# Optimization experiments

Measured on AMD Instinct MI355X. Metric: run time of the kernel, lower is better.

The kernel has to match this reference:

```python
import jax, jax.numpy as jnp
import numpy as np

N_NODES = 100000
N_EDGES = 3200000
D_FEAT = 128
N1 = 128
N2 = 64
NUM_CLASSES = 10
NUM_GRAPHS = 256


def gcn_conv(x, edge_index, W, b, num_nodes):
    """PyG GCNConv: y = D^-1/2 (A+I) D^-1/2 (x W) + b, self-loops added."""
    src, dst = edge_index[0], edge_index[1]
    # degree including self-loop (edge weight 1)
    deg = jax.ops.segment_sum(jnp.ones_like(dst, dtype=x.dtype), dst,
                              num_segments=num_nodes) + 1.0
    dis = jnp.where(deg > 0, deg ** -0.5, 0.0)  # deg_inv_sqrt, [N]
    h = x @ W                                    # transform first, [N, out]
    norm = dis[src] * dis[dst]                   # [E]
    msg = h[src] * norm[:, None]                 # gather + scale, [E, out]
    agg = jax.ops.segment_sum(msg, dst, num_segments=num_nodes)
    agg = agg + h * (dis * dis)[:, None]         # self-loop contribution
    return agg + b


def global_mean_pool(x, batch, num_graphs):
    sums = jax.ops.segment_sum(x, batch, num_segments=num_graphs)
    cnt = jax.ops.segment_sum(jnp.ones((x.shape[0],), dtype=x.dtype), batch,
                              num_segments=num_graphs)
    return sums / jnp.maximum(cnt, 1.0)[:, None]


def setup_inputs() -> dict:
    key = jax.random.key(0)
    ks = jax.random.split(key, 8)
    x = jax.random.normal(ks[0], (N_NODES, D_FEAT), dtype=jnp.float32)
    edge_index = jax.random.randint(ks[1], (2, N_EDGES), 0, N_NODES, dtype=jnp.int64)
    batch = jnp.sort(jax.random.randint(ks[2], (N_NODES,), 0, NUM_GRAPHS, dtype=jnp.int64))
    W1 = jax.random.normal(ks[3], (D_FEAT, N1), dtype=jnp.float32) / np.sqrt(D_FEAT)
    b1 = jnp.zeros((N1,), dtype=jnp.float32)
    W2 = jax.random.normal(ks[4], (N1, N2), dtype=jnp.float32) / np.sqrt(N1)
    b2 = jnp.zeros((N2,), dtype=jnp.float32)
    Wfc = jax.random.normal(ks[5], (N2, NUM_CLASSES), dtype=jnp.float32) / np.sqrt(N2)
    bfc = jnp.zeros((NUM_CLASSES,), dtype=jnp.float32)
    return {"x": x, "edge_index": edge_index, "batch": batch,
            "W1": W1, "b1": b1, "W2": W2, "b2": b2,
            "Wfc": Wfc, "bfc": bfc, "num_graphs": NUM_GRAPHS}


def reference(x, edge_index, batch, W1, b1, W2, b2, Wfc, bfc, num_graphs):
    n = x.shape[0]
    h = gcn_conv(x, edge_index, W1, b1, n)
    h = jax.nn.relu(h)
    h = gcn_conv(h, edge_index, W2, b2, n)
    g = global_mean_pool(h, batch, num_graphs)   # [num_graphs, N2]
    # dropout is identity at inference
    return g @ Wfc + bfc                          # [num_graphs, num_classes]
```

## Files before the change

### kernel.cpp

```cpp
#include <hip/hip_runtime.h>
#include <math.h>

typedef unsigned int  u32;
typedef unsigned short u16;

#define TILE1 8192
#define BKW   256
#define CAP   9216

typedef __attribute__((ext_vector_type(8))) short bf16x8;
typedef __attribute__((ext_vector_type(4))) float f32x4;
typedef __attribute__((ext_vector_type(2))) float f32x2;
union frag_u { bf16x8 v; u32 u[4]; uint4 q; };

__device__ inline u32 bf16_rne(float f) {
    u32 u = __float_as_uint(f);
    return (u + 0x7FFFu + ((u >> 16) & 1u)) >> 16;
}
__device__ inline float bf_lo(u32 u) { return __uint_as_float(u << 16); }
__device__ inline float bf_hi(u32 u) { return __uint_as_float(u & 0xFFFF0000u); }

__device__ inline f32x2 up2(u32 u) {
    f32x2 t;
    t.x = __uint_as_float(u << 16);
    t.y = __uint_as_float(u & 0xFFFF0000u);
    return t;
}
__device__ inline void add8p(f32x2* a, uint4 q) {
    a[0] += up2(q.x); a[1] += up2(q.y); a[2] += up2(q.z); a[3] += up2(q.w);
}

__device__ inline u32 relu_pk(u32 v) {
    u32 s = v & 0x80008000u;
    u32 m = (s >> 15) * 0xFFFFu;
    return v & ~m;
}


__global__ __launch_bounds__(512) void k_part1(const int* __restrict__ ei,
                                               int* __restrict__ bucketCur,
                                               u32* __restrict__ tmp,
                                               int E, int N, int NBK) {
    __shared__ int hist[2048];
    __shared__ int base[512];
    const int tid = threadIdx.x;
    if (tid < NBK) {
        hist[tid] = 0; hist[512 + tid] = 0;
        hist[1024 + tid] = 0; hist[1536 + tid] = 0;
    }
    __syncthreads();

    const int rep = (tid & 3) << 9;
    const int t0 = blockIdx.x * TILE1;
    const int4* ei4s = (const int4*)ei;
    const int4* ei4d = (const int4*)(ei + E);
    const int q0 = t0 >> 2;
    const int QE = E >> 2;

    int sv[16], dv[16], key[16];
#pragma unroll
    for (int j = 0; j < 4; ++j) {
        int qi = q0 + j * 512 + tid;
        int4 s4 = make_int4(0, 0, 0, 0), d4 = make_int4(-1, -1, -1, -1);
        if (qi < QE) { s4 = ei4s[qi]; d4 = ei4d[qi]; }
        sv[4 * j + 0] = s4.x; dv[4 * j + 0] = d4.x;
        sv[4 * j + 1] = s4.y; dv[4 * j + 1] = d4.y;
        sv[4 * j + 2] = s4.z; dv[4 * j + 2] = d4.z;
        sv[4 * j + 3] = s4.w; dv[4 * j + 3] = d4.w;
    }
#pragma unroll
    for (int j = 0; j < 16; ++j) {
        key[j] = -1;
        if ((unsigned)dv[j] < (unsigned)N && (unsigned)sv[j] < (unsigned)N) {
            key[j] = dv[j] >> 8;
            atomicAdd(&hist[key[j] + rep], 1);
        }
    }
    __syncthreads();
    if (tid < NBK) {
        int tot = hist[tid] + hist[512 + tid] + hist[1024 + tid] + hist[1536 + tid];
        base[tid] = atomicAdd(&bucketCur[tid], tot);
        hist[tid] = 0;
    }
    __syncthreads();
#pragma unroll
    for (int j = 0; j < 16; ++j) {
        if (key[j] >= 0) {
            int slot = atomicAdd(&hist[key[j]], 1);
            int off = base[key[j]] + slot;
            if (off < CAP)
                tmp[(size_t)key[j] * CAP + off] =
                    ((u32)(dv[j] & 255) << 17) | (u32)sv[j];
        }
    }
}

__global__ __launch_bounds__(512) void k_part2(const int* __restrict__ bucketCnt,
                                               const u32* __restrict__ tmp,
                                               int* __restrict__ csr,
                                               int* __restrict__ rowptr,
                                               float* __restrict__ dis,
                                               int N, int NBK) {
    __shared__ int hist[256];
    __shared__ int ts[512];
    __shared__ int sStart;
    const int b = blockIdx.x;
    const int t = threadIdx.x;

    int myCnt = (t < NBK) ? bucketCnt[t] : 0;
    ts[t] = myCnt;
    __syncthreads();
    for (int off = 1; off < 512; off <<= 1) {
        int u = (t >= off) ? ts[t - off] : 0;
        __syncthreads();
        ts[t] += u;
        __syncthreads();
    }
    if (t == b) sStart = ts[t] - myCnt;
    if (b == 0 && t == NBK - 1) rowptr[N] = ts[t];
    __syncthreads();
    const int start = sStart;
    const int cnt = bucketCnt[b];
    const u32* src = tmp + (size_t)b * CAP;

    if (t < 256) hist[t] = 0;
    __syncthreads();
    for (int i = t; i < cnt; i += 512)
        atomicAdd(&hist[src[i] >> 17], 1);
    __syncthreads();

    int h = (t < 256) ? hist[t] : 0;
    ts[t] = h;
    __syncthreads();
    for (int off = 1; off < 512; off <<= 1) {
        int u = (t >= off) ? ts[t - off] : 0;
        __syncthreads();
        ts[t] += u;
        __syncthreads();
    }
    if (t < 256) hist[t] = ts[t] - h;
    __syncthreads();

    if (t < 256) {
        int gn = (b << 8) + t;
        if (gn < N) {
            int e0 = hist[t];
            int e1 = (t < 255) ? hist[t + 1] : cnt;
            rowptr[gn] = start + e0;
            dis[gn] = rsqrtf((float)(e1 - e0) + 1.0f);
        }
    }
    __syncthreads();

    for (int i = t; i < cnt; i += 512) {
        u32 v = src[i];
        int p = atomicAdd(&hist[v >> 17], 1);
        csr[start + p] = (int)(v & 0x1FFFFu);
    }
}


__global__ __launch_bounds__(256) void k_convW(
    const float* __restrict__ W1, const float* __restrict__ W2,
    u32* __restrict__ W1h, u32* __restrict__ W1l,
    u32* __restrict__ W2h, u32* __restrict__ W2l,
    int* __restrict__ bucketCur, int NBK)
{
    int idx = blockIdx.x * 256 + threadIdx.x;
    if (idx < NBK) bucketCur[idx] = 0;
    if (idx < 8192) {
        int n = idx >> 6, k = (idx & 63) * 2;
        float w0 = W1[k * 128 + n], w1 = W1[(k + 1) * 128 + n];
        u32 h0 = bf16_rne(w0), h1 = bf16_rne(w1);
        u32 l0 = bf16_rne(w0 - __uint_as_float(h0 << 16));
        u32 l1 = bf16_rne(w1 - __uint_as_float(h1 << 16));
        W1h[idx] = h0 | (h1 << 16);
        W1l[idx] = l0 | (l1 << 16);
    } else if (idx < 12288) {
        int i2 = idx - 8192;
        int n = i2 >> 6, k = (i2 & 63) * 2;
        float w0 = W2[k * 64 + n], w1 = W2[(k + 1) * 64 + n];
        u32 h0 = bf16_rne(w0), h1 = bf16_rne(w1);
        u32 l0 = bf16_rne(w0 - __uint_as_float(h0 << 16));
        u32 l1 = bf16_rne(w1 - __uint_as_float(h1 << 16));
        W2h[i2] = h0 | (h1 << 16);
        W2l[i2] = l0 | (l1 << 16);
    }
}


__global__ __launch_bounds__(256) void k_gemm1m(
    const float* __restrict__ X, const u32* __restrict__ Wh,
    const u32* __restrict__ Wl, const float* __restrict__ dis,
    u32* __restrict__ Hb, int M)
{
    __shared__ uint4 sW[4096];
    const int tid = threadIdx.x;
    const uint4* Wh4 = (const uint4*)Wh;
    const uint4* Wl4 = (const uint4*)Wl;
#pragma unroll
    for (int i = 0; i < 8; ++i) {
        int idx = tid + i * 256;
        int l = idx >> 4, j = idx & 15;
        int js = j ^ (l & 7);
        sW[l * 16 + js] = Wh4[idx];
        sW[2048 + l * 16 + js] = Wl4[idx];
    }
    __syncthreads();

    const int w = tid >> 6, lane = tid & 63;
    const int mrow = blockIdx.x * 128 + w * 32;
    const int m16 = lane & 15, quad = lane >> 4;

    frag_u Ah[2][4], Al[2][4];
#pragma unroll
    for (int t = 0; t < 2; ++t) {
        int gm = mrow + t * 16 + m16; if (gm >= M) gm = M - 1;
        const float* xr = X + (size_t)gm * 128;
#pragma unroll
        for (int kt = 0; kt < 4; ++kt) {
            int kb = kt * 32 + quad * 8;
            float4 xa = *(const float4*)(xr + kb);
            float4 xb = *(const float4*)(xr + kb + 4);
            float xe[8] = {xa.x, xa.y, xa.z, xa.w, xb.x, xb.y, xb.z, xb.w};
#pragma unroll
            for (int j = 0; j < 4; ++j) {
                u32 h0 = bf16_rne(xe[2 * j]),     h1 = bf16_rne(xe[2 * j + 1]);
                u32 l0 = bf16_rne(xe[2 * j]     - __uint_as_float(h0 << 16));
                u32 l1 = bf16_rne(xe[2 * j + 1] - __uint_as_float(h1 << 16));
                Ah[t][kt].u[j] = h0 | (h1 << 16);
                Al[t][kt].u[j] = l0 | (l1 << 16);
            }
        }
    }

    float dv[2][4];
#pragma unroll
    for (int t = 0; t < 2; ++t)
#pragma unroll
        for (int r = 0; r < 4; ++r) {
            int gR = mrow + t * 16 + quad * 4 + r;
            dv[t][r] = (gR < M) ? dis[gR] : 0.f;
        }

#pragma unroll
    for (int nt = 0; nt < 8; ++nt) {
        f32x4 acc0 = {0.f, 0.f, 0.f, 0.f};
        f32x4 acc1 = {0.f, 0.f, 0.f, 0.f};
        int l = nt * 16 + m16;
        int swz = l & 7;
#pragma unroll
        for (int kt = 0; kt < 4; ++kt) {
            frag_u Bh, Bl;
            int jb = (kt * 4 + quad) ^ swz;
            Bh.q = sW[l * 16 + jb];
            Bl.q = sW[2048 + l * 16 + jb];
            acc0 = __builtin_amdgcn_mfma_f32_16x16x32_bf16(Al[0][kt].v, Bh.v, acc0, 0, 0, 0);
            acc0 = __builtin_amdgcn_mfma_f32_16x16x32_bf16(Ah[0][kt].v, Bl.v, acc0, 0, 0, 0);
            acc0 = __builtin_amdgcn_mfma_f32_16x16x32_bf16(Ah[0][kt].v, Bh.v, acc0, 0, 0, 0);
            acc1 = __builtin_amdgcn_mfma_f32_16x16x32_bf16(Al[1][kt].v, Bh.v, acc1, 0, 0, 0);
            acc1 = __builtin_amdgcn_mfma_f32_16x16x32_bf16(Ah[1][kt].v, Bl.v, acc1, 0, 0, 0);
            acc1 = __builtin_amdgcn_mfma_f32_16x16x32_bf16(Ah[1][kt].v, Bh.v, acc1, 0, 0, 0);
        }
#pragma unroll
        for (int r = 0; r < 4; ++r) {
            float vs0 = acc0[r] * dv[0][r];
            float vo0 = __shfl_xor(vs0, 1, 64);
            float vs1 = acc1[r] * dv[1][r];
            float vo1 = __shfl_xor(vs1, 1, 64);
            if ((m16 & 1) == 0) {
                int gR0 = mrow + quad * 4 + r;
                if (gR0 < M)
                    Hb[(size_t)gR0 * 64 + nt * 8 + (m16 >> 1)] =
                        bf16_rne(vs0) | (bf16_rne(vo0) << 16);
                int gR1 = mrow + 16 + quad * 4 + r;
                if (gR1 < M)
                    Hb[(size_t)gR1 * 64 + nt * 8 + (m16 >> 1)] =
                        bf16_rne(vs1) | (bf16_rne(vo1) << 16);
            }
        }
    }
}


__global__ __launch_bounds__(256) void k_gemm2m(
    const u32* __restrict__ Xb, const u32* __restrict__ Wh,
    const u32* __restrict__ Wl, const float* __restrict__ dis,
    u32* __restrict__ Hb, int M)
{
    __shared__ uint4 sW[2176];
    const int tid = threadIdx.x;
    const uint4* Wh4 = (const uint4*)Wh;
    const uint4* Wl4 = (const uint4*)Wl;
#pragma unroll
    for (int i = 0; i < 4; ++i) {
        int idx = tid + i * 256;
        int l = idx >> 4, j = idx & 15;
        sW[l * 17 + j] = Wh4[l * 16 + j];
        sW[1088 + l * 17 + j] = Wl4[l * 16 + j];
    }
    __syncthreads();

    const int w = tid >> 6, lane = tid & 63;
    const int mrow = blockIdx.x * 128 + w * 32;
    const int m16 = lane & 15, quad = lane >> 4;

    const uint4* X4 = (const uint4*)Xb;
    frag_u A[2][4];
#pragma unroll
    for (int t = 0; t < 2; ++t) {
        int gm = mrow + t * 16 + m16; if (gm >= M) gm = M - 1;
#pragma unroll
        for (int kt = 0; kt < 4; ++kt) {
            A[t][kt].q = X4[(size_t)gm * 16 + kt * 4 + quad];
#pragma unroll
            for (int j = 0; j < 4; ++j) A[t][kt].u[j] = relu_pk(A[t][kt].u[j]);
        }
    }

    float dv[2][4];
#pragma unroll
    for (int t = 0; t < 2; ++t)
#pragma unroll
        for (int r = 0; r < 4; ++r) {
            int gR = mrow + t * 16 + quad * 4 + r;
            dv[t][r] = (gR < M) ? dis[gR] : 0.f;
        }

#pragma unroll
    for (int nt = 0; nt < 4; ++nt) {
        f32x4 acc0 = {0.f, 0.f, 0.f, 0.f};
        f32x4 acc1 = {0.f, 0.f, 0.f, 0.f};
        int l = nt * 16 + m16;
#pragma unroll
        for (int kt = 0; kt < 4; ++kt) {
            frag_u Bh, Bl;
            Bh.q = sW[l * 17 + kt * 4 + quad];
            Bl.q = sW[1088 + l * 17 + kt * 4 + quad];
            acc0 = __builtin_amdgcn_mfma_f32_16x16x32_bf16(A[0][kt].v, Bl.v, acc0, 0, 0, 0);
            acc0 = __builtin_amdgcn_mfma_f32_16x16x32_bf16(A[0][kt].v, Bh.v, acc0, 0, 0, 0);
            acc1 = __builtin_amdgcn_mfma_f32_16x16x32_bf16(A[1][kt].v, Bl.v, acc1, 0, 0, 0);
            acc1 = __builtin_amdgcn_mfma_f32_16x16x32_bf16(A[1][kt].v, Bh.v, acc1, 0, 0, 0);
        }
#pragma unroll
        for (int r = 0; r < 4; ++r) {
            float vs0 = acc0[r] * dv[0][r];
            float vo0 = __shfl_xor(vs0, 1, 64);
            float vs1 = acc1[r] * dv[1][r];
            float vo1 = __shfl_xor(vs1, 1, 64);
            if ((m16 & 1) == 0) {
                int gR0 = mrow + quad * 4 + r;
                if (gR0 < M)
                    Hb[(size_t)gR0 * 32 + nt * 8 + (m16 >> 1)] =
                        bf16_rne(vs0) | (bf16_rne(vo0) << 16);
                int gR1 = mrow + 16 + quad * 4 + r;
                if (gR1 < M)
                    Hb[(size_t)gR1 * 32 + nt * 8 + (m16 >> 1)] =
                        bf16_rne(vs1) | (bf16_rne(vo1) << 16);
            }
        }
    }
}


template <int SH, int POFF>
__global__ __launch_bounds__(256) void k_aggh(
    const int* __restrict__ rowptr, const int* __restrict__ csr,
    const float* __restrict__ dis, const u32* __restrict__ Hb,
    const float* __restrict__ bias, u32* __restrict__ AGGb, int n0, int n1)
{
    int gid = blockIdx.x * 256 + threadIdx.x;
    int n = n0 + (gid >> 3);
    int li = threadIdx.x & 7;
    if (n >= n1) return;
    int e = rowptr[n];
    int s1 = rowptr[n + 1];
    const float dn = dis[n];
    const char* hb = (const char*)Hb;
    const u32 off = (u32)(POFF + li * 16);

    f32x2 acc[4];
#pragma unroll
    for (int j = 0; j < 4; ++j) acc[j] = 0.f;

    for (; e + 8 <= s1; e += 8) {
        u32 b0 = (u32)csr[e + 0] << SH;
        u32 b1 = (u32)csr[e + 1] << SH;
        u32 b2 = (u32)csr[e + 2] << SH;
        u32 b3 = (u32)csr[e + 3] << SH;
        u32 b4 = (u32)csr[e + 4] << SH;
        u32 b5 = (u32)csr[e + 5] << SH;
        u32 b6 = (u32)csr[e + 6] << SH;
        u32 b7 = (u32)csr[e + 7] << SH;
        uint4 q0 = *(const uint4*)(hb + b0 + off);
        uint4 q1 = *(const uint4*)(hb + b1 + off);
        uint4 q2 = *(const uint4*)(hb + b2 + off);
        uint4 q3 = *(const uint4*)(hb + b3 + off);
        uint4 q4 = *(const uint4*)(hb + b4 + off);
        uint4 q5 = *(const uint4*)(hb + b5 + off);
        uint4 q6 = *(const uint4*)(hb + b6 + off);
        uint4 q7 = *(const uint4*)(hb + b7 + off);
        add8p(acc, q0); add8p(acc, q1); add8p(acc, q2); add8p(acc, q3);
        add8p(acc, q4); add8p(acc, q5); add8p(acc, q6); add8p(acc, q7);
    }
    for (; e + 2 <= s1; e += 2) {
        u32 b0 = (u32)csr[e + 0] << SH;
        u32 b1 = (u32)csr[e + 1] << SH;
        uint4 q0 = *(const uint4*)(hb + b0 + off);
        uint4 q1 = *(const uint4*)(hb + b1 + off);
        add8p(acc, q0); add8p(acc, q1);
    }
    if (e < s1) {
        u32 b0 = (u32)csr[e] << SH;
        uint4 q0 = *(const uint4*)(hb + b0 + off);
        add8p(acc, q0);
    }
    {
        uint4 q = *(const uint4*)(hb + ((u32)n << SH) + off);
        add8p(acc, q);
    }

    float4 b0 = ((const float4*)bias)[POFF / 8 + li * 2 + 0];
    float4 b1 = ((const float4*)bias)[POFF / 8 + li * 2 + 1];
    uint4 p;
    p.x = bf16_rne(fmaf(dn, acc[0].x, b0.x)) | (bf16_rne(fmaf(dn, acc[0].y, b0.y)) << 16);
    p.y = bf16_rne(fmaf(dn, acc[1].x, b0.z)) | (bf16_rne(fmaf(dn, acc[1].y, b0.w)) << 16);
    p.z = bf16_rne(fmaf(dn, acc[2].x, b1.x)) | (bf16_rne(fmaf(dn, acc[2].y, b1.y)) << 16);
    p.w = bf16_rne(fmaf(dn, acc[3].x, b1.z)) | (bf16_rne(fmaf(dn, acc[3].y, b1.w)) << 16);
    ((uint4*)AGGb)[(size_t)n * (1 << (SH - 4)) + POFF / 16 + li] = p;
}


__device__ inline int lower_bound(const int* __restrict__ b, int n, int v) {
    int lo = 0, hi = n;
    while (lo < hi) { int m = (lo + hi) >> 1; if (b[m] < v) lo = m + 1; else hi = m; }
    return lo;
}

__global__ __launch_bounds__(256) void k_poolfc(
    const int* __restrict__ batch, const u32* __restrict__ AGGb2,
    const float* __restrict__ Wfc, const float* __restrict__ bfc,
    float* __restrict__ out, int n)
{
    int g = blockIdx.x;
    int start = lower_bound(batch, n, g);
    int end   = lower_bound(batch, n, g + 1);
    int tid = threadIdx.x;
    int f = tid & 63, stripe = tid >> 6;
    int ui = f >> 1, hi = f & 1;
    float acc = 0.f;
    for (int i = start + stripe; i < end; i += 4) {
        u32 v = AGGb2[(size_t)i * 32 + ui];
        acc += hi ? bf_hi(v) : bf_lo(v);
    }
    __shared__ float red[256];
    __shared__ float mean[64];
    red[tid] = acc;
    __syncthreads();
    if (tid < 64) {
        float s = red[tid] + red[tid + 64] + red[tid + 128] + red[tid + 192];
        float c = (float)(end - start);
        mean[tid] = s / fmaxf(c, 1.0f);
    }
    __syncthreads();
    if (tid < 10) {
        float o = bfc[tid];
        for (int k = 0; k < 64; ++k)
            o = fmaf(mean[k], Wfc[k * 10 + tid], o);
        out[g * 10 + tid] = o;
    }
}


extern "C" void kernel_launch(void* const* d_in, const int* in_sizes, int n_in,
                              void* d_out, int out_size, void* d_ws, size_t ws_size,
                              hipStream_t stream)
{
    const float* x    = (const float*)d_in[0];
    const int*   ei   = (const int*)d_in[1];
    const int*   batch= (const int*)d_in[2];
    const float* W1   = (const float*)d_in[3];
    const float* b1   = (const float*)d_in[4];
    const float* W2   = (const float*)d_in[5];
    const float* b2   = (const float*)d_in[6];
    const float* Wfc  = (const float*)d_in[7];
    const float* bfc  = (const float*)d_in[8];
    float* out = (float*)d_out;

    const int N  = in_sizes[0] / 128;
    const int E  = in_sizes[1] / 2;
    const int ng = out_size / 10;

    const int NBK = (N + BKW - 1) / BKW;
    const int NH  = N >> 1;

    int*   rowptr    = (int*)d_ws;
    int*   bucketCur = rowptr + 102400;
    float* dis       = (float*)(bucketCur + 512);
    int*   csr       = (int*)(dis + 102400);
    u32*   tmp       = (u32*)(csr + E);
    u32*   Hb1       = tmp;
    u32*   agg2b     = tmp;
    u32*   agg1b     = (u32*)((int*)tmp + (size_t)N * 64);
    u16*   Hb2       = (u16*)((int*)agg1b + (size_t)N * 128);
    u32*   W1h       = (u32*)((int*)Hb2 + (size_t)N * 32);
    u32*   W1l       = W1h + 8192;
    u32*   W2h       = W1l + 8192;
    u32*   W2l       = W2h + 4096;

    k_convW<<<48, 256, 0, stream>>>(W1, W2, W1h, W1l, W2h, W2l, bucketCur, NBK);
    k_part1<<<(E + TILE1 - 1) / TILE1, 512, 0, stream>>>(ei, bucketCur, tmp, E, N, NBK);
    k_part2<<<NBK, 512, 0, stream>>>(bucketCur, tmp, csr, rowptr, dis, N, NBK);

    k_gemm1m<<<(N + 127) / 128, 256, 0, stream>>>(x, W1h, W1l, dis, Hb1, N);
    k_aggh<8, 0><<<(NH * 8 + 255) / 256, 256, 0, stream>>>(rowptr, csr, dis, Hb1, b1, agg1b, 0, NH);
    k_aggh<8, 0><<<((N - NH) * 8 + 255) / 256, 256, 0, stream>>>(rowptr, csr, dis, Hb1, b1, agg1b, NH, N);
    k_aggh<8, 128><<<(NH * 8 + 255) / 256, 256, 0, stream>>>(rowptr, csr, dis, Hb1, b1, agg1b, 0, NH);
    k_aggh<8, 128><<<((N - NH) * 8 + 255) / 256, 256, 0, stream>>>(rowptr, csr, dis, Hb1, b1, agg1b, NH, N);

    k_gemm2m<<<(N + 127) / 128, 256, 0, stream>>>(agg1b, W2h, W2l, dis, (u32*)Hb2, N);
    k_aggh<7, 0><<<(NH * 8 + 255) / 256, 256, 0, stream>>>(rowptr, csr, dis, (const u32*)Hb2, b2, agg2b, 0, NH);
    k_aggh<7, 0><<<((N - NH) * 8 + 255) / 256, 256, 0, stream>>>(rowptr, csr, dis, (const u32*)Hb2, b2, agg2b, NH, N);

    k_poolfc<<<ng, 256, 0, stream>>>(batch, agg2b, Wfc, bfc, out, N);
}
```

Baseline: 414.1 us.

## Fuse layer-1 aggregation with layer-2 GEMM through shared memory

Replaces the four split layer-1 aggregation launches and the separate layer-2 GEMM with one kernel. Each block aggregates 64 nodes' 128-wide features into swizzled LDS, then runs the MFMA GEMM with W2 read straight from global memory. This drops the agg1 write/read round trip through HBM and several launches, and merges the split layer-2 aggregation launches into one. In exchange the gather and GEMM phases can no longer overlap across blocks, and the W2 fragments are now loaded from global memory instead of LDS.

```diff
diff --git a/kernel.cpp b/kernel.cpp
--- a/kernel.cpp
+++ b/kernel.cpp
@@ -283,80 +283,123 @@
 }
 
 
-__global__ __launch_bounds__(256) void k_gemm2m(
-    const u32* __restrict__ Xb, const u32* __restrict__ Wh,
-    const u32* __restrict__ Wl, const float* __restrict__ dis,
-    u32* __restrict__ Hb, int M)
+__global__ __launch_bounds__(256) void k_agg1g2(
+    const int* __restrict__ rowptr, const int* __restrict__ csr,
+    const float* __restrict__ dis, const u32* __restrict__ Hb1,
+    const float* __restrict__ b1,
+    const u32* __restrict__ W2h, const u32* __restrict__ W2l,
+    u32* __restrict__ Hb2, int N)
 {
-    __shared__ uint4 sW[2176];
+    __shared__ uint4 sH[1024];
     const int tid = threadIdx.x;
-    const uint4* Wh4 = (const uint4*)Wh;
-    const uint4* Wl4 = (const uint4*)Wl;
-#pragma unroll
-    for (int i = 0; i < 4; ++i) {
-        int idx = tid + i * 256;
-        int l = idx >> 4, j = idx & 15;
-        sW[l * 17 + j] = Wh4[l * 16 + j];
-        sW[1088 + l * 17 + j] = Wl4[l * 16 + j];
-    }
-    __syncthreads();
-
-    const int w = tid >> 6, lane = tid & 63;
-    const int mrow = blockIdx.x * 128 + w * 32;
-    const int m16 = lane & 15, quad = lane >> 4;
-
-    const uint4* X4 = (const uint4*)Xb;
-    frag_u A[2][4];
-#pragma unroll
-    for (int t = 0; t < 2; ++t) {
-        int gm = mrow + t * 16 + m16; if (gm >= M) gm = M - 1;
+    const int n0 = blockIdx.x * 64;
+    const char* hb = (const char*)Hb1;
+    const int grp = tid >> 3, li = tid & 7;
+
+    for (int it = 0; it < 4; ++it) {
+        int task = it * 32 + grp;
+        int half = task & 1;
+        int nl = task >> 1;
+        int n = n0 + nl;
+        uint4 p = make_uint4(0u, 0u, 0u, 0u);
+        if (n < N) {
+            int e = rowptr[n];
+            int s1 = rowptr[n + 1];
+            const float dn = dis[n];
+            const u32 off = (u32)(half * 128 + li * 16);
+
+            f32x2 acc[4];
+#pragma unroll
+            for (int j = 0; j < 4; ++j) acc[j] = 0.f;
+
+            for (; e + 8 <= s1; e += 8) {
+                u32 a0 = (u32)csr[e + 0] << 8; u32 a1 = (u32)csr[e + 1] << 8;
+                u32 a2 = (u32)csr[e + 2] << 8; u32 a3 = (u32)csr[e + 3] << 8;
+                u32 a4 = (u32)csr[e + 4] << 8; u32 a5 = (u32)csr[e + 5] << 8;
+                u32 a6 = (u32)csr[e + 6] << 8; u32 a7 = (u32)csr[e + 7] << 8;
+                uint4 q0 = *(const uint4*)(hb + a0 + off);
+                uint4 q1 = *(const uint4*)(hb + a1 + off);
+                uint4 q2 = *(const uint4*)(hb + a2 + off);
+                uint4 q3 = *(const uint4*)(hb + a3 + off);
+                uint4 q4 = *(const uint4*)(hb + a4 + off);
+                uint4 q5 = *(const uint4*)(hb + a5 + off);
+                uint4 q6 = *(const uint4*)(hb + a6 + off);
+                uint4 q7 = *(const uint4*)(hb + a7 + off);
+                add8p(acc, q0); add8p(acc, q1); add8p(acc, q2); add8p(acc, q3);
+                add8p(acc, q4); add8p(acc, q5); add8p(acc, q6); add8p(acc, q7);
+            }
+            for (; e + 2 <= s1; e += 2) {
+                u32 a0 = (u32)csr[e + 0] << 8; u32 a1 = (u32)csr[e + 1] << 8;
+                uint4 q0 = *(const uint4*)(hb + a0 + off);
+                uint4 q1 = *(const uint4*)(hb + a1 + off);
+                add8p(acc, q0); add8p(acc, q1);
+            }
+            if (e < s1) {
+                u32 a0 = (u32)csr[e] << 8;
+                uint4 q0 = *(const uint4*)(hb + a0 + off);
+                add8p(acc, q0);
+            }
+            {
+                uint4 q = *(const uint4*)(hb + ((u32)n << 8) + off);
+                add8p(acc, q);
+            }
+
+            float4 bb0 = ((const float4*)b1)[(half * 128 + li * 16) >> 3];
+            float4 bb1 = ((const float4*)b1)[((half * 128 + li * 16) >> 3) + 1];
+            p.x = bf16_rne(fmaf(dn, acc[0].x, bb0.x)) | (bf16_rne(fmaf(dn, acc[0].y, bb0.y)) << 16);
+            p.y = bf16_rne(fmaf(dn, acc[1].x, bb0.z)) | (bf16_rne(fmaf(dn, acc[1].y, bb0.w)) << 16);
+            p.z = bf16_rne(fmaf(dn, acc[2].x, bb1.x)) | (bf16_rne(fmaf(dn, acc[2].y, bb1.y)) << 16);
+            p.w = bf16_rne(fmaf(dn, acc[3].x, bb1.z)) | (bf16_rne(fmaf(dn, acc[3].y, bb1.w)) << 16);
+        }
+        sH[nl * 16 + ((half * 8 + li) ^ (nl & 7))] = p;
+    }
+    __syncthreads();
+
+    {
+        const int w = tid >> 6, lane = tid & 63;
+        const int m16 = lane & 15, quad = lane >> 4;
+        const uint4* Wh4 = (const uint4*)W2h;
+        const uint4* Wl4 = (const uint4*)W2l;
+        const int mrow = n0 + w * 16;
+        const int gl = w * 16 + m16;
+
+        frag_u A[4];
 #pragma unroll
         for (int kt = 0; kt < 4; ++kt) {
-            A[t][kt].q = X4[(size_t)gm * 16 + kt * 4 + quad];
-#pragma unroll
-            for (int j = 0; j < 4; ++j) A[t][kt].u[j] = relu_pk(A[t][kt].u[j]);
-        }
-    }
-
-    float dv[2][4];
-#pragma unroll
-    for (int t = 0; t < 2; ++t)
+            A[kt].q = sH[gl * 16 + ((kt * 4 + quad) ^ (gl & 7))];
+#pragma unroll
+            for (int j = 0; j < 4; ++j) A[kt].u[j] = relu_pk(A[kt].u[j]);
+        }
+
+        float dv[4];
 #pragma unroll
         for (int r = 0; r < 4; ++r) {
-            int gR = mrow + t * 16 + quad * 4 + r;
-            dv[t][r] = (gR < M) ? dis[gR] : 0.f;
-        }
-
-#pragma unroll
-    for (int nt = 0; nt < 4; ++nt) {
-        f32x4 acc0 = {0.f, 0.f, 0.f, 0.f};
-        f32x4 acc1 = {0.f, 0.f, 0.f, 0.f};
-        int l = nt * 16 + m16;
-#pragma unroll
-        for (int kt = 0; kt < 4; ++kt) {
-            frag_u Bh, Bl;
-            Bh.q = sW[l * 17 + kt * 4 + quad];
-            Bl.q = sW[1088 + l * 17 + kt * 4 + quad];
-            acc0 = __builtin_amdgcn_mfma_f32_16x16x32_bf16(A[0][kt].v, Bl.v, acc0, 0, 0, 0);
-            acc0 = __builtin_amdgcn_mfma_f32_16x16x32_bf16(A[0][kt].v, Bh.v, acc0, 0, 0, 0);
-            acc1 = __builtin_amdgcn_mfma_f32_16x16x32_bf16(A[1][kt].v, Bl.v, acc1, 0, 0, 0);
-            acc1 = __builtin_amdgcn_mfma_f32_16x16x32_bf16(A[1][kt].v, Bh.v, acc1, 0, 0, 0);
-        }
-#pragma unroll
-        for (int r = 0; r < 4; ++r) {
-            float vs0 = acc0[r] * dv[0][r];
-            float vo0 = __shfl_xor(vs0, 1, 64);
-            float vs1 = acc1[r] * dv[1][r];
-            float vo1 = __shfl_xor(vs1, 1, 64);
-            if ((m16 & 1) == 0) {
-                int gR0 = mrow + quad * 4 + r;
-                if (gR0 < M)
-                    Hb[(size_t)gR0 * 32 + nt * 8 + (m16 >> 1)] =
-                        bf16_rne(vs0) | (bf16_rne(vo0) << 16);
-                int gR1 = mrow + 16 + quad * 4 + r;
-                if (gR1 < M)
-                    Hb[(size_t)gR1 * 32 + nt * 8 + (m16 >> 1)] =
-                        bf16_rne(vs1) | (bf16_rne(vo1) << 16);
+            int gR = mrow + quad * 4 + r;
+            dv[r] = (gR < N) ? dis[gR] : 0.f;
+        }
+
+#pragma unroll
+        for (int nt = 0; nt < 4; ++nt) {
+            f32x4 acc = {0.f, 0.f, 0.f, 0.f};
+            int l = nt * 16 + m16;
+#pragma unroll
+            for (int kt = 0; kt < 4; ++kt) {
+                frag_u Bh, Bl;
+                Bh.q = Wh4[l * 16 + kt * 4 + quad];
+                Bl.q = Wl4[l * 16 + kt * 4 + quad];
+                acc = __builtin_amdgcn_mfma_f32_16x16x32_bf16(A[kt].v, Bl.v, acc, 0, 0, 0);
+                acc = __builtin_amdgcn_mfma_f32_16x16x32_bf16(A[kt].v, Bh.v, acc, 0, 0, 0);
+            }
+#pragma unroll
+            for (int r = 0; r < 4; ++r) {
+                float vs = acc[r] * dv[r];
+                float vo = __shfl_xor(vs, 1, 64);
+                if ((m16 & 1) == 0) {
+                    int gR = mrow + quad * 4 + r;
+                    if (gR < N)
+                        Hb2[(size_t)gR * 32 + nt * 8 + (m16 >> 1)] =
+                            bf16_rne(vs) | (bf16_rne(vo) << 16);
+                }
             }
         }
     }
@@ -367,12 +410,12 @@
 __global__ __launch_bounds__(256) void k_aggh(
     const int* __restrict__ rowptr, const int* __restrict__ csr,
     const float* __restrict__ dis, const u32* __restrict__ Hb,
-    const float* __restrict__ bias, u32* __restrict__ AGGb, int n0, int n1)
+    const float* __restrict__ bias, u32* __restrict__ AGGb, int N)
 {
     int gid = blockIdx.x * 256 + threadIdx.x;
-    int n = n0 + (gid >> 3);
+    int n = gid >> 3;
     int li = threadIdx.x & 7;
-    if (n >= n1) return;
+    if (n >= N) return;
     int e = rowptr[n];
     int s1 = rowptr[n + 1];
     const float dn = dis[n];
@@ -384,35 +427,30 @@
     for (int j = 0; j < 4; ++j) acc[j] = 0.f;
 
     for (; e + 8 <= s1; e += 8) {
-        u32 b0 = (u32)csr[e + 0] << SH;
-        u32 b1 = (u32)csr[e + 1] << SH;
-        u32 b2 = (u32)csr[e + 2] << SH;
-        u32 b3 = (u32)csr[e + 3] << SH;
-        u32 b4 = (u32)csr[e + 4] << SH;
-        u32 b5 = (u32)csr[e + 5] << SH;
-        u32 b6 = (u32)csr[e + 6] << SH;
-        u32 b7 = (u32)csr[e + 7] << SH;
-        uint4 q0 = *(const uint4*)(hb + b0 + off);
-        uint4 q1 = *(const uint4*)(hb + b1 + off);
-        uint4 q2 = *(const uint4*)(hb + b2 + off);
-        uint4 q3 = *(const uint4*)(hb + b3 + off);
-        uint4 q4 = *(const uint4*)(hb + b4 + off);
-        uint4 q5 = *(const uint4*)(hb + b5 + off);
-        uint4 q6 = *(const uint4*)(hb + b6 + off);
-        uint4 q7 = *(const uint4*)(hb + b7 + off);
+        u32 a0 = (u32)csr[e + 0] << SH; u32 a1 = (u32)csr[e + 1] << SH;
+        u32 a2 = (u32)csr[e + 2] << SH; u32 a3 = (u32)csr[e + 3] << SH;
+        u32 a4 = (u32)csr[e + 4] << SH; u32 a5 = (u32)csr[e + 5] << SH;
+        u32 a6 = (u32)csr[e + 6] << SH; u32 a7 = (u32)csr[e + 7] << SH;
+        uint4 q0 = *(const uint4*)(hb + a0 + off);
+        uint4 q1 = *(const uint4*)(hb + a1 + off);
+        uint4 q2 = *(const uint4*)(hb + a2 + off);
+        uint4 q3 = *(const uint4*)(hb + a3 + off);
+        uint4 q4 = *(const uint4*)(hb + a4 + off);
+        uint4 q5 = *(const uint4*)(hb + a5 + off);
+        uint4 q6 = *(const uint4*)(hb + a6 + off);
+        uint4 q7 = *(const uint4*)(hb + a7 + off);
         add8p(acc, q0); add8p(acc, q1); add8p(acc, q2); add8p(acc, q3);
         add8p(acc, q4); add8p(acc, q5); add8p(acc, q6); add8p(acc, q7);
     }
     for (; e + 2 <= s1; e += 2) {
-        u32 b0 = (u32)csr[e + 0] << SH;
-        u32 b1 = (u32)csr[e + 1] << SH;
-        uint4 q0 = *(const uint4*)(hb + b0 + off);
-        uint4 q1 = *(const uint4*)(hb + b1 + off);
+        u32 a0 = (u32)csr[e + 0] << SH; u32 a1 = (u32)csr[e + 1] << SH;
+        uint4 q0 = *(const uint4*)(hb + a0 + off);
+        uint4 q1 = *(const uint4*)(hb + a1 + off);
         add8p(acc, q0); add8p(acc, q1);
     }
     if (e < s1) {
-        u32 b0 = (u32)csr[e] << SH;
-        uint4 q0 = *(const uint4*)(hb + b0 + off);
+        u32 a0 = (u32)csr[e] << SH;
+        uint4 q0 = *(const uint4*)(hb + a0 + off);
         add8p(acc, q0);
     }
     {
@@ -420,13 +458,13 @@
         add8p(acc, q);
     }
 
-    float4 b0 = ((const float4*)bias)[POFF / 8 + li * 2 + 0];
-    float4 b1 = ((const float4*)bias)[POFF / 8 + li * 2 + 1];
+    float4 bb0 = ((const float4*)bias)[POFF / 8 + li * 2 + 0];
+    float4 bb1 = ((const float4*)bias)[POFF / 8 + li * 2 + 1];
     uint4 p;
-    p.x = bf16_rne(fmaf(dn, acc[0].x, b0.x)) | (bf16_rne(fmaf(dn, acc[0].y, b0.y)) << 16);
-    p.y = bf16_rne(fmaf(dn, acc[1].x, b0.z)) | (bf16_rne(fmaf(dn, acc[1].y, b0.w)) << 16);
-    p.z = bf16_rne(fmaf(dn, acc[2].x, b1.x)) | (bf16_rne(fmaf(dn, acc[2].y, b1.y)) << 16);
-    p.w = bf16_rne(fmaf(dn, acc[3].x, b1.z)) | (bf16_rne(fmaf(dn, acc[3].y, b1.w)) << 16);
+    p.x = bf16_rne(fmaf(dn, acc[0].x, bb0.x)) | (bf16_rne(fmaf(dn, acc[0].y, bb0.y)) << 16);
+    p.y = bf16_rne(fmaf(dn, acc[1].x, bb0.z)) | (bf16_rne(fmaf(dn, acc[1].y, bb0.w)) << 16);
+    p.z = bf16_rne(fmaf(dn, acc[2].x, bb1.x)) | (bf16_rne(fmaf(dn, acc[2].y, bb1.y)) << 16);
+    p.w = bf16_rne(fmaf(dn, acc[3].x, bb1.z)) | (bf16_rne(fmaf(dn, acc[3].y, bb1.w)) << 16);
     ((uint4*)AGGb)[(size_t)n * (1 << (SH - 4)) + POFF / 16 + li] = p;
 }
 
@@ -492,7 +530,6 @@
     const int ng = out_size / 10;
 
     const int NBK = (N + BKW - 1) / BKW;
-    const int NH  = N >> 1;
 
     int*   rowptr    = (int*)d_ws;
     int*   bucketCur = rowptr + 102400;
@@ -500,9 +537,8 @@
     int*   csr       = (int*)(dis + 102400);
     u32*   tmp       = (u32*)(csr + E);
     u32*   Hb1       = tmp;
-    u32*   agg2b     = tmp;
-    u32*   agg1b     = (u32*)((int*)tmp + (size_t)N * 64);
-    u16*   Hb2       = (u16*)((int*)agg1b + (size_t)N * 128);
+    u32*   agg2b    = (u32*)((int*)tmp + (size_t)N * 64);
+    u16*   Hb2       = (u16*)((int*)agg2b + (size_t)N * 32);
     u32*   W1h       = (u32*)((int*)Hb2 + (size_t)N * 32);
     u32*   W1l       = W1h + 8192;
     u32*   W2h       = W1l + 8192;
@@ -513,14 +549,12 @@
     k_part2<<<NBK, 512, 0, stream>>>(bucketCur, tmp, csr, rowptr, dis, N, NBK);
 
     k_gemm1m<<<(N + 127) / 128, 256, 0, stream>>>(x, W1h, W1l, dis, Hb1, N);
-    k_aggh<8, 0><<<(NH * 8 + 255) / 256, 256, 0, stream>>>(rowptr, csr, dis, Hb1, b1, agg1b, 0, NH);
-    k_aggh<8, 0><<<((N - NH) * 8 + 255) / 256, 256, 0, stream>>>(rowptr, csr, dis, Hb1, b1, agg1b, NH, N);
-    k_aggh<8, 128><<<(NH * 8 + 255) / 256, 256, 0, stream>>>(rowptr, csr, dis, Hb1, b1, agg1b, 0, NH);
-    k_aggh<8, 128><<<((N - NH) * 8 + 255) / 256, 256, 0, stream>>>(rowptr, csr, dis, Hb1, b1, agg1b, NH, N);
-
-    k_gemm2m<<<(N + 127) / 128, 256, 0, stream>>>(agg1b, W2h, W2l, dis, (u32*)Hb2, N);
-    k_aggh<7, 0><<<(NH * 8 + 255) / 256, 256, 0, stream>>>(rowptr, csr, dis, (const u32*)Hb2, b2, agg2b, 0, NH);
-    k_aggh<7, 0><<<((N - NH) * 8 + 255) / 256, 256, 0, stream>>>(rowptr, csr, dis, (const u32*)Hb2, b2, agg2b, NH, N);
+
+    k_agg1g2<<<(N + 63) / 64, 256, 0, stream>>>(rowptr, csr, dis, Hb1, b1,
+                                                W2h, W2l, (u32*)Hb2, N);
+
+    k_aggh<7, 0><<<(N * 8 + 255) / 256, 256, 0, stream>>>(rowptr, csr, dis,
+                                                          (const u32*)Hb2, b2, agg2b, N);
 
     k_poolfc<<<ng, 256, 0, stream>>>(batch, agg2b, Wfc, bfc, out, N);
 }
```

New measurement: 403.8 us. -2.5%, faster.

## Store transformed node features in FP8 and aggregate in single full-width pass

Applied to the files above, without the earlier changes.

The GEMM outputs (x·W scaled by deg^-1/2) are now packed as FP8 pairs instead of bf16, halving the bytes gathered per edge in the sparse aggregation. Because rows are smaller, each layer's aggregation becomes a single launch covering all features, replacing the split half-node and half-feature launches. This cuts random gather traffic, which dominates with 3.2M edges. FP8 has far less mantissa and range than bf16, so accuracy may fall outside the tolerance.

```diff
diff --git a/kernel.cpp b/kernel.cpp
--- a/kernel.cpp
+++ b/kernel.cpp
@@ -26,8 +26,23 @@
     t.y = __uint_as_float(u & 0xFFFF0000u);
     return t;
 }
-__device__ inline void add8p(f32x2* a, uint4 q) {
-    a[0] += up2(q.x); a[1] += up2(q.y); a[2] += up2(q.z); a[3] += up2(q.w);
+
+__device__ inline u16 fp8pk(float a, float b) {
+    return (u16)(__builtin_amdgcn_cvt_pk_fp8_f32(a, b, 0, false) & 0xFFFF);
+}
+__device__ inline f32x2 pk8lo(u32 w) {
+    f32x2 r = __builtin_amdgcn_cvt_pk_f32_fp8(w, false);
+    return r;
+}
+__device__ inline f32x2 pk8hi(u32 w) {
+    f32x2 r = __builtin_amdgcn_cvt_pk_f32_fp8(w, true);
+    return r;
+}
+__device__ inline void add16p(f32x2* a, uint4 q) {
+    a[0] += pk8lo(q.x); a[1] += pk8hi(q.x);
+    a[2] += pk8lo(q.y); a[3] += pk8hi(q.y);
+    a[4] += pk8lo(q.z); a[5] += pk8hi(q.z);
+    a[6] += pk8lo(q.w); a[7] += pk8hi(q.w);
 }
 
 __device__ inline u32 relu_pk(u32 v) {
@@ -192,7 +207,7 @@
 __global__ __launch_bounds__(256) void k_gemm1m(
     const float* __restrict__ X, const u32* __restrict__ Wh,
     const u32* __restrict__ Wl, const float* __restrict__ dis,
-    u32* __restrict__ Hb, int M)
+    u16* __restrict__ Hb, int M)
 {
     __shared__ uint4 sW[4096];
     const int tid = threadIdx.x;
@@ -271,12 +286,10 @@
             if ((m16 & 1) == 0) {
                 int gR0 = mrow + quad * 4 + r;
                 if (gR0 < M)
-                    Hb[(size_t)gR0 * 64 + nt * 8 + (m16 >> 1)] =
-                        bf16_rne(vs0) | (bf16_rne(vo0) << 16);
+                    Hb[(size_t)gR0 * 64 + nt * 8 + (m16 >> 1)] = fp8pk(vs0, vo0);
                 int gR1 = mrow + 16 + quad * 4 + r;
                 if (gR1 < M)
-                    Hb[(size_t)gR1 * 64 + nt * 8 + (m16 >> 1)] =
-                        bf16_rne(vs1) | (bf16_rne(vo1) << 16);
+                    Hb[(size_t)gR1 * 64 + nt * 8 + (m16 >> 1)] = fp8pk(vs1, vo1);
             }
         }
     }
@@ -286,7 +299,7 @@
 __global__ __launch_bounds__(256) void k_gemm2m(
     const u32* __restrict__ Xb, const u32* __restrict__ Wh,
     const u32* __restrict__ Wl, const float* __restrict__ dis,
-    u32* __restrict__ Hb, int M)
+    u16* __restrict__ Hb, int M)
 {
     __shared__ uint4 sW[2176];
     const int tid = threadIdx.x;
@@ -351,83 +364,83 @@
             if ((m16 & 1) == 0) {
                 int gR0 = mrow + quad * 4 + r;
                 if (gR0 < M)
-                    Hb[(size_t)gR0 * 32 + nt * 8 + (m16 >> 1)] =
-                        bf16_rne(vs0) | (bf16_rne(vo0) << 16);
+                    Hb[(size_t)gR0 * 32 + nt * 8 + (m16 >> 1)] = fp8pk(vs0, vo0);
                 int gR1 = mrow + 16 + quad * 4 + r;
                 if (gR1 < M)
-                    Hb[(size_t)gR1 * 32 + nt * 8 + (m16 >> 1)] =
-                        bf16_rne(vs1) | (bf16_rne(vo1) << 16);
+                    Hb[(size_t)gR1 * 32 + nt * 8 + (m16 >> 1)] = fp8pk(vs1, vo1);
             }
         }
     }
 }
 
 
-template <int SH, int POFF>
-__global__ __launch_bounds__(256) void k_aggh(
+template <int LGS, int SH>
+__global__ __launch_bounds__(256) void k_aggf(
     const int* __restrict__ rowptr, const int* __restrict__ csr,
-    const float* __restrict__ dis, const u32* __restrict__ Hb,
-    const float* __restrict__ bias, u32* __restrict__ AGGb, int n0, int n1)
+    const float* __restrict__ dis, const u16* __restrict__ Hb,
+    const float* __restrict__ bias, u32* __restrict__ AGGb, int N)
 {
+    const int LG = 1 << LGS;
+    const int OUT4 = 1 << (SH - 3);
     int gid = blockIdx.x * 256 + threadIdx.x;
-    int n = n0 + (gid >> 3);
-    int li = threadIdx.x & 7;
-    if (n >= n1) return;
+    int n = gid >> LGS;
+    int li = threadIdx.x & (LG - 1);
+    if (n >= N) return;
     int e = rowptr[n];
     int s1 = rowptr[n + 1];
     const float dn = dis[n];
     const char* hb = (const char*)Hb;
-    const u32 off = (u32)(POFF + li * 16);
-
-    f32x2 acc[4];
-#pragma unroll
-    for (int j = 0; j < 4; ++j) acc[j] = 0.f;
+    const u32 off = (u32)li << 4;
+
+    f32x2 acc[8];
+#pragma unroll
+    for (int j = 0; j < 8; ++j) acc[j] = 0.f;
 
     for (; e + 8 <= s1; e += 8) {
-        u32 b0 = (u32)csr[e + 0] << SH;
-        u32 b1 = (u32)csr[e + 1] << SH;
-        u32 b2 = (u32)csr[e + 2] << SH;
-        u32 b3 = (u32)csr[e + 3] << SH;
-        u32 b4 = (u32)csr[e + 4] << SH;
-        u32 b5 = (u32)csr[e + 5] << SH;
-        u32 b6 = (u32)csr[e + 6] << SH;
-        u32 b7 = (u32)csr[e + 7] << SH;
-        uint4 q0 = *(const uint4*)(hb + b0 + off);
-        uint4 q1 = *(const uint4*)(hb + b1 + off);
-        uint4 q2 = *(const uint4*)(hb + b2 + off);
-        uint4 q3 = *(const uint4*)(hb + b3 + off);
-        uint4 q4 = *(const uint4*)(hb + b4 + off);
-        uint4 q5 = *(const uint4*)(hb + b5 + off);
-        uint4 q6 = *(const uint4*)(hb + b6 + off);
-        uint4 q7 = *(const uint4*)(hb + b7 + off);
-        add8p(acc, q0); add8p(acc, q1); add8p(acc, q2); add8p(acc, q3);
-        add8p(acc, q4); add8p(acc, q5); add8p(acc, q6); add8p(acc, q7);
+        u32 a0 = (u32)csr[e + 0] << SH; u32 a1 = (u32)csr[e + 1] << SH;
+        u32 a2 = (u32)csr[e + 2] << SH; u32 a3 = (u32)csr[e + 3] << SH;
+        u32 a4 = (u32)csr[e + 4] << SH; u32 a5 = (u32)csr[e + 5] << SH;
+        u32 a6 = (u32)csr[e + 6] << SH; u32 a7 = (u32)csr[e + 7] << SH;
+        uint4 q0 = *(const uint4*)(hb + a0 + off);
+        uint4 q1 = *(const uint4*)(hb + a1 + off);
+        uint4 q2 = *(const uint4*)(hb + a2 + off);
+        uint4 q3 = *(const uint4*)(hb + a3 + off);
+        uint4 q4 = *(const uint4*)(hb + a4 + off);
+        uint4 q5 = *(const uint4*)(hb + a5 + off);
+        uint4 q6 = *(const uint4*)(hb + a6 + off);
+        uint4 q7 = *(const uint4*)(hb + a7 + off);
+        add16p(acc, q0); add16p(acc, q1); add16p(acc, q2); add16p(acc, q3);
+        add16p(acc, q4); add16p(acc, q5); add16p(acc, q6); add16p(acc, q7);
     }
     for (; e + 2 <= s1; e += 2) {
-        u32 b0 = (u32)csr[e + 0] << SH;
-        u32 b1 = (u32)csr[e + 1] << SH;
-        uint4 q0 = *(const uint4*)(hb + b0 + off);
-        uint4 q1 = *(const uint4*)(hb + b1 + off);
-        add8p(acc, q0); add8p(acc, q1);
+        u32 a0 = (u32)csr[e + 0] << SH; u32 a1 = (u32)csr[e + 1] << SH;
+        uint4 q0 = *(const uint4*)(hb + a0 + off);
+        uint4 q1 = *(const uint4*)(hb + a1 + off);
+        add16p(acc, q0); add16p(acc, q1);
     }
     if (e < s1) {
-        u32 b0 = (u32)csr[e] << SH;
-        uint4 q0 = *(const uint4*)(hb + b0 + off);
-        add8p(acc, q0);
+        u32 a0 = (u32)csr[e] << SH;
+        uint4 q0 = *(const uint4*)(hb + a0 + off);
+        add16p(acc, q0);
     }
     {
         uint4 q = *(const uint4*)(hb + ((u32)n << SH) + off);
-        add8p(acc, q);
-    }
-
-    float4 b0 = ((const float4*)bias)[POFF / 8 + li * 2 + 0];
-    float4 b1 = ((const float4*)bias)[POFF / 8 + li * 2 + 1];
-    uint4 p;
-    p.x = bf16_rne(fmaf(dn, acc[0].x, b0.x)) | (bf16_rne(fmaf(dn, acc[0].y, b0.y)) << 16);
-    p.y = bf16_rne(fmaf(dn, acc[1].x, b0.z)) | (bf16_rne(fmaf(dn, acc[1].y, b0.w)) << 16);
-    p.z = bf16_rne(fmaf(dn, acc[2].x, b1.x)) | (bf16_rne(fmaf(dn, acc[2].y, b1.y)) << 16);
-    p.w = bf16_rne(fmaf(dn, acc[3].x, b1.z)) | (bf16_rne(fmaf(dn, acc[3].y, b1.w)) << 16);
-    ((uint4*)AGGb)[(size_t)n * (1 << (SH - 4)) + POFF / 16 + li] = p;
+        add16p(acc, q);
+    }
+
+    const float4* bb = (const float4*)bias + li * 4;
+    float4 b0_ = bb[0], b1_ = bb[1], b2_ = bb[2], b3_ = bb[3];
+    uint4 p0, p1;
+    p0.x = bf16_rne(fmaf(dn, acc[0].x, b0_.x)) | (bf16_rne(fmaf(dn, acc[0].y, b0_.y)) << 16);
+    p0.y = bf16_rne(fmaf(dn, acc[1].x, b0_.z)) | (bf16_rne(fmaf(dn, acc[1].y, b0_.w)) << 16);
+    p0.z = bf16_rne(fmaf(dn, acc[2].x, b1_.x)) | (bf16_rne(fmaf(dn, acc[2].y, b1_.y)) << 16);
+    p0.w = bf16_rne(fmaf(dn, acc[3].x, b1_.z)) | (bf16_rne(fmaf(dn, acc[3].y, b1_.w)) << 16);
+    p1.x = bf16_rne(fmaf(dn, acc[4].x, b2_.x)) | (bf16_rne(fmaf(dn, acc[4].y, b2_.y)) << 16);
+    p1.y = bf16_rne(fmaf(dn, acc[5].x, b2_.z)) | (bf16_rne(fmaf(dn, acc[5].y, b2_.w)) << 16);
+    p1.z = bf16_rne(fmaf(dn, acc[6].x, b3_.x)) | (bf16_rne(fmaf(dn, acc[6].y, b3_.y)) << 16);
+    p1.w = bf16_rne(fmaf(dn, acc[7].x, b3_.z)) | (bf16_rne(fmaf(dn, acc[7].y, b3_.w)) << 16);
+    ((uint4*)AGGb)[(size_t)n * OUT4 + li * 2 + 0] = p0;
+    ((uint4*)AGGb)[(size_t)n * OUT4 + li * 2 + 1] = p1;
 }
 
 
@@ -492,14 +505,13 @@
     const int ng = out_size / 10;
 
     const int NBK = (N + BKW - 1) / BKW;
-    const int NH  = N >> 1;
 
     int*   rowptr    = (int*)d_ws;
     int*   bucketCur = rowptr + 102400;
     float* dis       = (float*)(bucketCur + 512);
     int*   csr       = (int*)(dis + 102400);
     u32*   tmp       = (u32*)(csr + E);
-    u32*   Hb1       = tmp;
+    u16*   Hb1       = (u16*)tmp;
     u32*   agg2b     = tmp;
     u32*   agg1b     = (u32*)((int*)tmp + (size_t)N * 64);
     u16*   Hb2       = (u16*)((int*)agg1b + (size_t)N * 128);
@@ -513,14 +525,10 @@
     k_part2<<<NBK, 512, 0, stream>>>(bucketCur, tmp, csr, rowptr, dis, N, NBK);
 
     k_gemm1m<<<(N + 127) / 128, 256, 0, stream>>>(x, W1h, W1l, dis, Hb1, N);
-    k_aggh<8, 0><<<(NH * 8 + 255) / 256, 256, 0, stream>>>(rowptr, csr, dis, Hb1, b1, agg1b, 0, NH);
-    k_aggh<8, 0><<<((N - NH) * 8 + 255) / 256, 256, 0, stream>>>(rowptr, csr, dis, Hb1, b1, agg1b, NH, N);
-    k_aggh<8, 128><<<(NH * 8 + 255) / 256, 256, 0, stream>>>(rowptr, csr, dis, Hb1, b1, agg1b, 0, NH);
-    k_aggh<8, 128><<<((N - NH) * 8 + 255) / 256, 256, 0, stream>>>(rowptr, csr, dis, Hb1, b1, agg1b, NH, N);
-
-    k_gemm2m<<<(N + 127) / 128, 256, 0, stream>>>(agg1b, W2h, W2l, dis, (u32*)Hb2, N);
-    k_aggh<7, 0><<<(NH * 8 + 255) / 256, 256, 0, stream>>>(rowptr, csr, dis, (const u32*)Hb2, b2, agg2b, 0, NH);
-    k_aggh<7, 0><<<((N - NH) * 8 + 255) / 256, 256, 0, stream>>>(rowptr, csr, dis, (const u32*)Hb2, b2, agg2b, NH, N);
+    k_aggf<3, 7><<<(N * 8 + 255) / 256, 256, 0, stream>>>(rowptr, csr, dis, Hb1, b1, agg1b, N);
+
+    k_gemm2m<<<(N + 127) / 128, 256, 0, stream>>>(agg1b, W2h, W2l, dis, Hb2, N);
+    k_aggf<2, 6><<<(N * 4 + 255) / 256, 256, 0, stream>>>(rowptr, csr, dis, Hb2, b2, agg2b, N);
 
     k_poolfc<<<ng, 256, 0, stream>>>(batch, agg2b, Wfc, bfc, out, N);
 }
```

New measurement: 338.3 us. -18.3%, faster.
